# Optimization experiments

Hardware: AMD Instinct MI355X
Metric: run time of the kernel (lower is better)

## Reference

```python
import jax, jax.numpy as jnp
import numpy as np

N_QUBITS = 14
N_LAYERS = 2
LATENT_DIM = 14
DIM = 2 ** N_QUBITS
PAIRS = [(i, i + 1) for i in range(N_QUBITS - 1)]  # 'linear' entanglement


def _cnot_perm(control, target, n):
    # permutation of basis indices implementing CNOT(control, target)
    idx = np.arange(2 ** n)
    cbit = (idx >> (n - control - 1)) & 1
    flipped = np.where(cbit == 1, idx ^ (1 << (n - target - 1)), idx)
    return jnp.asarray(flipped)

CNOT_PERMS = [_cnot_perm(c, t, N_QUBITS) for c, t in PAIRS]


def _apply_1q(state, gate, q):
    # state: (B, 2^n) complex; gate: (2,2) or (B,2,2) complex
    B = state.shape[0]
    s = state.reshape(B, 2 ** (N_QUBITS - q - 1), 2, 2 ** q)
    if gate.ndim == 2:
        s = jnp.einsum('ij,bkjl->bkil', gate, s)
    else:
        s = jnp.einsum('bij,bkjl->bkil', gate, s)
    return s.reshape(B, DIM)


def _ry_batched(theta):
    c = jnp.cos(theta / 2)
    s = jnp.sin(theta / 2)
    g = jnp.stack([jnp.stack([c, -s], -1), jnp.stack([s, c], -1)], -2)  # (B,2,2)
    return g.astype(jnp.complex64)


def _ry(theta):
    c = jnp.cos(theta / 2)
    s = jnp.sin(theta / 2)
    return jnp.stack([jnp.stack([c, -s]), jnp.stack([s, c])]).astype(jnp.complex64)


def _rz(theta):
    th = theta.astype(jnp.complex64)
    e0 = jnp.exp(-0.5j * th)
    e1 = jnp.exp(0.5j * th)
    zero = jnp.zeros((), jnp.complex64)
    return jnp.stack([jnp.stack([e0, zero]), jnp.stack([zero, e1])])


def setup_inputs() -> dict:
    key = jax.random.key(0)
    k1, k2 = jax.random.split(key)
    latent = jax.random.normal(k1, (256, LATENT_DIM), dtype=jnp.float32)
    weights = jax.random.normal(k2, (N_LAYERS * N_QUBITS * 3,), dtype=jnp.float32) * 0.1
    return {"latent": latent, "weights": weights}


def reference(latent, weights):
    B = latent.shape[0]
    state = jnp.zeros((B, DIM), dtype=jnp.complex64).at[:, 0].set(1.0)
    # latent encoding: RY(pi * z_i) on qubit i
    for i in range(min(LATENT_DIM, N_QUBITS)):
        state = _apply_1q(state, _ry_batched(latent[:, i] * np.pi), i)
    # variational layers
    for layer in range(N_LAYERS):
        off = layer * N_QUBITS * 3
        for q in range(N_QUBITS):
            b = off + q * 3
            state = _apply_1q(state, _ry(weights[b]), q)
            state = _apply_1q(state, _rz(weights[b + 1]), q)
            state = _apply_1q(state, _ry(weights[b + 2]), q)
        for perm in CNOT_PERMS:
            state = state[:, perm]
    return jnp.abs(state) ** 2
```

## Files before the change

kernel.cpp:

```cpp
#include <hip/hip_runtime.h>


typedef float f32x2 __attribute__((ext_vector_type(2)));

constexpr int NQ    = 14;
constexpr int DIM   = 1 << NQ;
constexpr int NT    = 256;
constexpr int SPLIT = 4;
constexpr int CHUNK = DIM / SPLIT;

__device__ __forceinline__ f32x2 cmul(f32x2 a, f32x2 b) {
    return f32x2{a.x * b.x - a.y * b.y, a.x * b.y + a.y * b.x};
}
__device__ __forceinline__ int g7(int x)  { return x ^ (x >> 1); }
__device__ __forceinline__ int g7i(int x) { x ^= x >> 1; x ^= x >> 2; x ^= x >> 4; return x; }

__global__ __launch_bounds__(NT)
void qsim_kernel(const float* __restrict__ latent,
                 const float* __restrict__ weights,
                 float* __restrict__ out)
{
    __shared__ f32x2 vq [2 * NQ];
    __shared__ f32x2 m1 [4 * NQ];
    __shared__ f32x2 plo[128], phi[128];
    __shared__ f32x2 cc0[128], cc1[128], dd0[128], dd1[128];
    __shared__ float4 fj[128];
    __shared__ float4 eA[128];

    const int b   = blockIdx.x >> 2;
    const int qtr = blockIdx.x & 3;
    const int tid = threadIdx.x;

    if (tid < NQ) {
        const int q = tid;
        const float a = weights[3 * q] + 3.14159265358979323846f * latent[b * NQ + q];
        const float t = weights[3 * q + 1];
        const float c = weights[3 * q + 2];
        const float ct = cosf(0.5f * t),       stt = sinf(0.5f * t);
        const float cp = cosf(0.5f * (a + c)), sp  = sinf(0.5f * (a + c));
        const float cm = cosf(0.5f * (a - c)), sm  = sinf(0.5f * (a - c));
        vq[2 * q + 0] = f32x2{ct * cp, -stt * cm};
        vq[2 * q + 1] = f32x2{ct * sp,  stt * sm};
    } else if (tid >= 64 && tid < 64 + NQ) {
        const int q = tid - 64;
        const float a = weights[3 * NQ + 3 * q];
        const float t = weights[3 * NQ + 3 * q + 1];
        const float c = weights[3 * NQ + 3 * q + 2];
        const float ct = cosf(0.5f * t),       stt = sinf(0.5f * t);
        const float cp = cosf(0.5f * (a + c)), sp  = sinf(0.5f * (a + c));
        const float cm = cosf(0.5f * (a - c)), sm  = sinf(0.5f * (a - c));
        m1[4 * q + 0] = f32x2{ ct * cp, -stt * cm};
        m1[4 * q + 1] = f32x2{-ct * sp,  stt * sm};
        m1[4 * q + 2] = f32x2{ ct * sp,  stt * sm};
        m1[4 * q + 3] = f32x2{ ct * cp,  stt * cm};
    }
    __syncthreads();

    {
        const int half = tid >> 7;
        const int m    = tid & 127;
        const int qb   = half * 7;
        f32x2 p = {1.0f, 0.0f};
        #pragma unroll
        for (int j = 0; j < 7; ++j)
            p = cmul(p, vq[2 * (qb + j) + ((m >> j) & 1)]);
        (half ? phi : plo)[m] = p;
    }
    __syncthreads();

    {
        const int w    = tid >> 6;
        const int lane = tid & 63;
        const int u0 = 2 * lane, u1 = 2 * lane + 1;

        f32x2 r0, r1;
        if (w == 0)      { r0 = plo[g7(u0)];       r1 = plo[g7(u1)];       }
        else if (w == 1) { r0 = plo[g7(u0) ^ 64];  r1 = plo[g7(u1) ^ 64];  }
        else if (w == 2) { r0 = phi[g7(u0)];       r1 = f32x2{0.f, 0.f};   }
        else             { r0 = f32x2{0.f, 0.f};   r1 = phi[g7(u1)];       }

        const int mbase = (w >> 1) * 7;

        {
            const f32x2 M00 = m1[4 * mbase + 0], M01 = m1[4 * mbase + 1];
            const f32x2 M10 = m1[4 * mbase + 2], M11 = m1[4 * mbase + 3];
            const f32x2 n0 = cmul(M00, r0) + cmul(M01, r1);
            const f32x2 n1 = cmul(M10, r0) + cmul(M11, r1);
            r0 = n0; r1 = n1;
        }
        #pragma unroll
        for (int k = 1; k < 7; ++k) {
            const int q = mbase + k;
            const f32x2 M00 = m1[4 * q + 0], M01 = m1[4 * q + 1];
            const f32x2 M10 = m1[4 * q + 2], M11 = m1[4 * q + 3];
            const int msk = 1 << (k - 1);
            const int bit = (lane >> (k - 1)) & 1;
            f32x2 p0, p1;
            p0.x = __shfl_xor(r0.x, msk, 64); p0.y = __shfl_xor(r0.y, msk, 64);
            p1.x = __shfl_xor(r1.x, msk, 64); p1.y = __shfl_xor(r1.y, msk, 64);
            const f32x2 lo0 = bit ? p0 : r0, hi0 = bit ? r0 : p0;
            const f32x2 lo1 = bit ? p1 : r1, hi1 = bit ? r1 : p1;
            const f32x2 Ma  = bit ? M10 : M00;
            const f32x2 Mb  = bit ? M11 : M01;
            r0 = cmul(Ma, lo0) + cmul(Mb, hi0);
            r1 = cmul(Ma, lo1) + cmul(Mb, hi1);
        }
        const int j0 = g7i(u0), j1 = g7i(u1);
        if (w == 0)      { cc0[j0] = r0; cc0[j1] = r1; }
        else if (w == 1) { cc1[j0] = r0; cc1[j1] = r1; }
        else if (w == 2) { dd0[j0] = r0; dd0[j1] = r1; }
        else             { dd1[j0] = r0; dd1[j1] = r1; }
    }
    __syncthreads();

    if (tid < 128) {
        const int j = tid;
        const f32x2 c0 = cc0[j], c1 = cc1[j];
        fj[j] = make_float4(c0.x * c0.x + c0.y * c0.y,
                            c1.x * c1.x + c1.y * c1.y,
                            c0.x * c1.x + c0.y * c1.y,
                            c0.y * c1.x - c0.x * c1.y);
    } else {
        const int A = tid - 128;
        const f32x2 d0 = dd0[A], d1 = dd1[A];
        eA[A] = make_float4(d0.x * d0.x + d0.y * d0.y,
                            d1.x * d1.x + d1.y * d1.y,
                            2.0f * (d0.x * d1.x + d0.y * d1.y),
                           -2.0f * (d0.y * d1.x - d0.x * d1.y));
    }
    __syncthreads();

    float* outb = out + (size_t)b * DIM + qtr * CHUNK;
    #pragma unroll
    for (int k = 0; k < CHUNK / NT; ++k) {
        const int ll = tid + k * NT;
        const int l  = qtr * CHUNK + ll;
        const int A  = l >> 7;
        const int j  = (l & 127) ^ ((A & 1) ? 127 : 0);
        const float4 e = eA[A];
        const float4 f = fj[j];
        outb[ll] = e.x * f.x + e.y * f.y + e.z * f.z + e.w * f.w;
    }
}

extern "C" void kernel_launch(void* const* d_in, const int* in_sizes, int n_in,
                              void* d_out, int out_size, void* d_ws, size_t ws_size,
                              hipStream_t stream) {
    const float* latent  = (const float*)d_in[0];
    const float* weights = (const float*)d_in[1];
    float* out = (float*)d_out;

    const int B = in_sizes[0] / NQ;
    qsim_kernel<<<B * SPLIT, NT, 0, stream>>>(latent, weights, out);
}
```

Measured before the change: 13.11 us.

## Vectorize output stores with SoA f-table, 512-thread blocks, fast sincos

Each batch element is now split across two 512-thread blocks instead of four 256-thread blocks. The final outer-product stage is restructured so that each thread loads four consecutive f-values from a structure-of-arrays layout and writes float4 outputs. Rows with odd A store their four values reversed, which keeps the index-reversal pattern. Precise sinf/cosf calls are replaced with __sincosf intrinsics. The aim is to cut the number of store instructions and the cost of the prologue, at the price of lower trig accuracy and idle threads during the setup phases.

```diff
diff --git a/kernel.cpp b/kernel.cpp
--- a/kernel.cpp
+++ b/kernel.cpp
@@ -2,12 +2,12 @@
 
 
 typedef float f32x2 __attribute__((ext_vector_type(2)));
+typedef float f32x4 __attribute__((ext_vector_type(4)));
 
 constexpr int NQ    = 14;
 constexpr int DIM   = 1 << NQ;
-constexpr int NT    = 256;
-constexpr int SPLIT = 4;
-constexpr int CHUNK = DIM / SPLIT;
+constexpr int NT    = 512;
+constexpr int SPLIT = 2;
 
 __device__ __forceinline__ f32x2 cmul(f32x2 a, f32x2 b) {
     return f32x2{a.x * b.x - a.y * b.y, a.x * b.y + a.y * b.x};
@@ -24,11 +24,11 @@
     __shared__ f32x2 m1 [4 * NQ];
     __shared__ f32x2 plo[128], phi[128];
     __shared__ f32x2 cc0[128], cc1[128], dd0[128], dd1[128];
-    __shared__ float4 fj[128];
-    __shared__ float4 eA[128];
+    __shared__ __align__(16) float fjx[128], fjy[128], fjz[128], fjw[128];
+    __shared__ f32x4 eA[128];
 
-    const int b   = blockIdx.x >> 2;
-    const int qtr = blockIdx.x & 3;
+    const int b   = blockIdx.x >> 1;
+    const int qtr = blockIdx.x & 1;
     const int tid = threadIdx.x;
 
     if (tid < NQ) {
@@ -36,9 +36,10 @@
         const float a = weights[3 * q] + 3.14159265358979323846f * latent[b * NQ + q];
         const float t = weights[3 * q + 1];
         const float c = weights[3 * q + 2];
-        const float ct = cosf(0.5f * t),       stt = sinf(0.5f * t);
-        const float cp = cosf(0.5f * (a + c)), sp  = sinf(0.5f * (a + c));
-        const float cm = cosf(0.5f * (a - c)), sm  = sinf(0.5f * (a - c));
+        float ct, stt, cp, sp, cm, sm;
+        __sincosf(0.5f * t, &stt, &ct);
+        __sincosf(0.5f * (a + c), &sp, &cp);
+        __sincosf(0.5f * (a - c), &sm, &cm);
         vq[2 * q + 0] = f32x2{ct * cp, -stt * cm};
         vq[2 * q + 1] = f32x2{ct * sp,  stt * sm};
     } else if (tid >= 64 && tid < 64 + NQ) {
@@ -46,9 +47,10 @@
         const float a = weights[3 * NQ + 3 * q];
         const float t = weights[3 * NQ + 3 * q + 1];
         const float c = weights[3 * NQ + 3 * q + 2];
-        const float ct = cosf(0.5f * t),       stt = sinf(0.5f * t);
-        const float cp = cosf(0.5f * (a + c)), sp  = sinf(0.5f * (a + c));
-        const float cm = cosf(0.5f * (a - c)), sm  = sinf(0.5f * (a - c));
+        float ct, stt, cp, sp, cm, sm;
+        __sincosf(0.5f * t, &stt, &ct);
+        __sincosf(0.5f * (a + c), &sp, &cp);
+        __sincosf(0.5f * (a - c), &sm, &cm);
         m1[4 * q + 0] = f32x2{ ct * cp, -stt * cm};
         m1[4 * q + 1] = f32x2{-ct * sp,  stt * sm};
         m1[4 * q + 2] = f32x2{ ct * sp,  stt * sm};
@@ -56,7 +58,7 @@
     }
     __syncthreads();
 
-    {
+    if (tid < 256) {
         const int half = tid >> 7;
         const int m    = tid & 127;
         const int qb   = half * 7;
@@ -68,7 +70,7 @@
     }
     __syncthreads();
 
-    {
+    if (tid < 256) {
         const int w    = tid >> 6;
         const int lane = tid & 63;
         const int u0 = 2 * lane, u1 = 2 * lane + 1;
@@ -116,30 +118,42 @@
     if (tid < 128) {
         const int j = tid;
         const f32x2 c0 = cc0[j], c1 = cc1[j];
-        fj[j] = make_float4(c0.x * c0.x + c0.y * c0.y,
-                            c1.x * c1.x + c1.y * c1.y,
-                            c0.x * c1.x + c0.y * c1.y,
-                            c0.y * c1.x - c0.x * c1.y);
-    } else {
+        fjx[j] = c0.x * c0.x + c0.y * c0.y;
+        fjy[j] = c1.x * c1.x + c1.y * c1.y;
+        fjz[j] = c0.x * c1.x + c0.y * c1.y;
+        fjw[j] = c0.y * c1.x - c0.x * c1.y;
+    } else if (tid < 256) {
         const int A = tid - 128;
         const f32x2 d0 = dd0[A], d1 = dd1[A];
-        eA[A] = make_float4(d0.x * d0.x + d0.y * d0.y,
-                            d1.x * d1.x + d1.y * d1.y,
-                            2.0f * (d0.x * d1.x + d0.y * d1.y),
-                           -2.0f * (d0.y * d1.x - d0.x * d1.y));
+        eA[A] = f32x4{d0.x * d0.x + d0.y * d0.y,
+                      d1.x * d1.x + d1.y * d1.y,
+                      2.0f * (d0.x * d1.x + d0.y * d1.y),
+                     -2.0f * (d0.y * d1.x - d0.x * d1.y)};
     }
     __syncthreads();
 
-    float* outb = out + (size_t)b * DIM + qtr * CHUNK;
-    #pragma unroll
-    for (int k = 0; k < CHUNK / NT; ++k) {
-        const int ll = tid + k * NT;
-        const int l  = qtr * CHUNK + ll;
-        const int A  = l >> 7;
-        const int j  = (l & 127) ^ ((A & 1) ? 127 : 0);
-        const float4 e = eA[A];
-        const float4 f = fj[j];
-        outb[ll] = e.x * f.x + e.y * f.y + e.z * f.z + e.w * f.w;
+    {
+        const int w    = tid >> 6;
+        const int lane = tid & 63;
+        const int h    = lane >> 5;
+        const int s    = lane & 31;
+
+        const f32x4 fx = *(const f32x4*)&fjx[4 * s];
+        const f32x4 fy = *(const f32x4*)&fjy[4 * s];
+        const f32x4 fz = *(const f32x4*)&fjz[4 * s];
+        const f32x4 fw = *(const f32x4*)&fjw[4 * s];
+
+        const int row0 = qtr * 64 + 8 * w + h;
+        const int col  = h ? (124 - 4 * s) : (4 * s);
+        float* op = out + (size_t)b * DIM + row0 * 128 + col;
+
+        #pragma unroll
+        for (int t = 0; t < 4; ++t) {
+            const f32x4 e = eA[row0 + 2 * t];
+            f32x4 o = e.x * fx + e.y * fy + e.z * fz + e.w * fw;
+            if (h) o = f32x4{o.w, o.z, o.y, o.x};
+            *(f32x4*)(op + t * 256) = o;
+        }
     }
 }
 
```

After: 11.56 us. -11.8%, faster.
